# Kernel optimization log

Measured on AMD Instinct MI355X. Metric: run time of the kernel, lower is better.

Reference implementation:

```python
import jax, jax.numpy as jnp
import numpy as np
import math

N = 60000          # nodes per node type
M = 60000          # edges per edge type
H = 64             # hidden_dim
PE = 4             # pe_dim
L = 3              # message passing layers
E = 24             # edge types
PE_LEN = 2 * N     # pe table length = 2 * num_pick_nodes
T = 6              # node types: object, ssBox, place_frame, ssCylinder, pick, place

# (src_type, dst_type) index per edge type, following detailed_edge_types order
SRC = np.array([0,1,2,1,2,0,4,5,0,1,2,3,0,4,2,4,3,4,0,5,3,5,2,5])
DST = np.array([1,0,1,2,0,2,5,4,0,1,2,3,4,0,4,2,4,3,5,0,5,3,5,2])


def posenc(n, d):
    pos = jnp.arange(n, dtype=jnp.float32)[:, None]
    div = jnp.exp(jnp.arange(0, d, 2, dtype=jnp.float32) * (-math.log(10000.0) / d))
    ang = pos * div  # [n, d//2]
    return jnp.stack([jnp.sin(ang), jnp.cos(ang)], axis=-1).reshape(n, d)


def setup_inputs():
    key = jax.random.key(0)
    ks = iter(jax.random.split(key, 48))
    def n_(shape, fan):
        return jax.random.normal(next(ks), shape, dtype=jnp.float32) / np.sqrt(fan).astype(np.float32)
    def ti(shape, hi):
        return jax.random.randint(next(ks), shape, 0, hi, dtype=jnp.int32)
    inp = {}
    inp['x_object'] = jax.random.normal(next(ks), (N, 4), dtype=jnp.float32)
    inp['x_ssBox'] = jax.random.normal(next(ks), (N, 4), dtype=jnp.float32)
    inp['x_place_frame'] = jax.random.normal(next(ks), (N, 4), dtype=jnp.float32)
    inp['x_ssCylinder'] = jax.random.normal(next(ks), (N, 3), dtype=jnp.float32)
    for nt in ['object', 'ssBox', 'place_frame', 'ssCylinder', 'pick', 'place']:
        inp['times_' + nt] = ti((N,), PE_LEN)
    inp['edge_index'] = ti((E, 2, M), N)
    inp['W_object'] = n_((8, H), 8); inp['b_object'] = jnp.zeros((H,), jnp.float32)
    inp['W_ssBox'] = n_((8, H), 8); inp['b_ssBox'] = jnp.zeros((H,), jnp.float32)
    inp['W_place_frame'] = n_((8, H), 8); inp['b_place_frame'] = jnp.zeros((H,), jnp.float32)
    inp['W_ssCylinder'] = n_((7, H), 7); inp['b_ssCylinder'] = jnp.zeros((H,), jnp.float32)
    inp['W_pick'] = n_((PE, H), PE); inp['b_pick'] = jnp.zeros((H,), jnp.float32)
    inp['W_place'] = n_((PE, H), PE); inp['b_place'] = jnp.zeros((H,), jnp.float32)
    inp['Wl'] = n_((L, E, H, H), H)
    inp['bl'] = jnp.zeros((L, E, H), jnp.float32)
    inp['Wr'] = n_((L, E, H, H), H)
    inp['Wm1'] = n_((H, H // 4), H); inp['bm1'] = jnp.zeros((H // 4,), jnp.float32)
    inp['Wm2'] = n_((H // 4, 1), H // 4); inp['bm2'] = jnp.zeros((1,), jnp.float32)
    return inp


def _forward(x_object, x_ssBox, x_place_frame, x_ssCylinder,
             W_object, b_object, W_ssBox, b_ssBox, W_place_frame, b_place_frame,
             W_ssCylinder, b_ssCylinder, W_pick, b_pick, W_place, b_place,
             Wl, bl, Wr, Wm1, bm1, Wm2, bm2,
             times_object, times_ssBox, times_place_frame, times_ssCylinder,
             times_pick, times_place, edge_index):
    pe = posenc(PE_LEN, PE)
    def emb(x, t, W, b):  # features || pe[times] -> linear
        return jnp.concatenate([x, pe[t]], axis=1) @ W + b
    X = jnp.stack([
        emb(x_object, times_object, W_object, b_object),
        emb(x_ssBox, times_ssBox, W_ssBox, b_ssBox),
        emb(x_place_frame, times_place_frame, W_place_frame, b_place_frame),
        emb(x_ssCylinder, times_ssCylinder, W_ssCylinder, b_ssCylinder),
        pe[times_pick] @ W_pick + b_pick,    # constraint nodes: pe -> linear
        pe[times_place] @ W_place + b_place,
    ])  # [T, N, H]

    src_e = edge_index[:, 0]  # [E, M]
    dst_e = edge_index[:, 1]  # [E, M]
    seg_sum = jax.vmap(lambda v, s: jax.ops.segment_sum(v, s, num_segments=N))
    counts = seg_sum(jnp.ones((E, M), jnp.float32), dst_e)  # [E, N] in-degree per edge type
    denom = jnp.maximum(counts, 1.0)[..., None]

    for l in range(L):
        # gather src node states per edge type: [E, M, H]
        msgs = jnp.take_along_axis(X[SRC], src_e[..., None], axis=1)
        # mean aggregation into dst nodes per edge type (SAGEConv aggr='mean')
        agg = seg_sum(msgs, dst_e) / denom  # [E, N, H]
        # out = lin_l(agg) + lin_r(x_dst) per edge type
        out_et = (jnp.einsum('enh,ehk->enk', agg, Wl[l]) + bl[l][:, None, :]
                  + jnp.einsum('enh,ehk->enk', X[DST], Wr[l]))  # [E, N, H]
        # sum contributions across edge types sharing a dst node type
        X = jax.ops.segment_sum(out_et, DST, num_segments=T)
        X = jax.nn.relu(X)

    # pool constraint (pick/place) node embeddings into a graph embedding
    graph_emb = X[4].sum(axis=0) + X[5].sum(axis=0)  # [H]
    h = jax.nn.relu(graph_emb)          # OutputMLP: act, (dropout=id), linear
    h = jax.nn.relu(h @ Wm1 + bm1)
    return h @ Wm2 + bm2                # [output_dim]


def reference(x_object, x_ssBox, x_place_frame, x_ssCylinder,
              times_object, times_ssBox, times_place_frame, times_ssCylinder,
              times_pick, times_place, edge_index,
              W_object, b_object, W_ssBox, b_ssBox, W_place_frame, b_place_frame,
              W_ssCylinder, b_ssCylinder, W_pick, b_pick, W_place, b_place,
              Wl, bl, Wr, Wm1, bm1, Wm2, bm2):
    return _forward(x_object, x_ssBox, x_place_frame, x_ssCylinder,
                    W_object, b_object, W_ssBox, b_ssBox, W_place_frame, b_place_frame,
                    W_ssCylinder, b_ssCylinder, W_pick, b_pick, W_place, b_place,
                    Wl, bl, Wr, Wm1, bm1, Wm2, bm2,
                    times_object, times_ssBox, times_place_frame, times_ssCylinder,
                    times_pick, times_place, edge_index)
```

## Files before the change

kernel.cpp:

```cpp
#include <hip/hip_runtime.h>


#define NN 60000
#define MM 60000
#define EE 24
#define TT 6
#define NTILES ((NN + 63) / 64)
#define SCH 2048
#define SNB ((NN + SCH - 1) / SCH)
#define CSRCAP 180

typedef unsigned short u16;
typedef unsigned int   u32;
typedef __attribute__((ext_vector_type(8))) short bf16x8;
typedef __attribute__((ext_vector_type(4))) float f32x4;

__constant__ int c_SRC[EE] = {0,1,2,1,2,0,4,5,0,1,2,3,0,4,2,4,3,4,0,5,3,5,2,5};
__constant__ int c_ELIST[TT][5] = {{1,4,8,13,19},{0,2,9,0,0},{3,5,10,15,23},
                                   {11,17,21,0,0},{7,12,14,16,0},{6,18,20,22,0}};
__constant__ int c_ECOUNT[TT] = {5,3,5,3,4,4};
__constant__ int c_TLIST[3][6] = {{0,1,2,3,4,5},{0,2,3,4,5,0},{4,5,0,0,0,0}};

__device__ __forceinline__ float lo16(u32 u){ union{u32 i; float f;} x; x.i = u << 16; return x.f; }
__device__ __forceinline__ float hi16(u32 u){ union{u32 i; float f;} x; x.i = u & 0xFFFF0000u; return x.f; }
__device__ __forceinline__ float bf2f(u16 u){ union{u32 i; float f;} x; x.i = (u32)u << 16; return x.f; }
__device__ __forceinline__ u16 f2bf(float f){
  union{float f; u32 i;} x; x.f = f;
  u32 r = (x.i + 0x7FFFu + ((x.i >> 16) & 1u)) >> 16;
  return (u16)r;
}
__device__ __forceinline__ u32 pack2(float a, float b){ return (u32)f2bf(a) | ((u32)f2bf(b) << 16); }

__global__ __launch_bounds__(256) void k_prep(const float* __restrict__ Wl, const float* __restrict__ bl,
                                              const float* __restrict__ Wr,
                                              u16* __restrict__ WlT, u16* __restrict__ WrTs,
                                              float* __restrict__ blsum)
{
  const int total1 = 3*EE*4096, total2 = 3*TT*4096, total3 = 3*TT*64;
  for (int i = blockIdx.x*blockDim.x + threadIdx.x; i < total1+total2+total3; i += gridDim.x*blockDim.x) {
    if (i < total1) {
      int h = i & 63, ko = (i >> 6) & 63, le = i >> 12;
      WlT[i] = f2bf(Wl[(size_t)le*4096 + h*64 + ko]);
    } else if (i < total1 + total2) {
      int j = i - total1;
      int h = j & 63, ko = (j >> 6) & 63, lt = j >> 12;
      int l = lt / TT, t = lt % TT;
      float s = 0.f;
      for (int q = 0; q < c_ECOUNT[t]; ++q) {
        int e = c_ELIST[t][q];
        s += Wr[((size_t)(l*EE + e)*64 + h)*64 + ko];
      }
      WrTs[j] = f2bf(s);
    } else {
      int j = i - total1 - total2;
      int k = j & 63, lt = j >> 6;
      int l = lt / TT, t = lt % TT;
      float s = 0.f;
      for (int q = 0; q < c_ECOUNT[t]; ++q) s += bl[(size_t)(l*EE + c_ELIST[t][q])*64 + k];
      blsum[j] = s;
    }
  }
}

__global__ __launch_bounds__(256) void k_pe(
    const int* __restrict__ tm0, const int* __restrict__ tm1,
    const int* __restrict__ tm2, const int* __restrict__ tm3,
    const int* __restrict__ tm4, const int* __restrict__ tm5,
    float4* __restrict__ pe)
{
  const int i = blockIdx.x*blockDim.x + threadIdx.x;
  if (i >= TT*NN) return;
  const int t = i / NN, n = i - t*NN;
  int tm;
  switch (t) {
    case 0:  tm = tm0[n]; break;
    case 1:  tm = tm1[n]; break;
    case 2:  tm = tm2[n]; break;
    case 3:  tm = tm3[n]; break;
    case 4:  tm = tm4[n]; break;
    default: tm = tm5[n]; break;
  }
  const float a0 = (float)tm, a1 = a0 * 0.01f;
  float4 v;
  v.x = sinf(a0); v.y = cosf(a0); v.z = sinf(a1); v.w = cosf(a1);
  pe[i] = v;
}

__global__ __launch_bounds__(256) void k_embed(
    const float* __restrict__ x0, const float* __restrict__ x1,
    const float* __restrict__ x2, const float* __restrict__ x3,
    const float4* __restrict__ pe,
    const float* __restrict__ W0, const float* __restrict__ b0,
    const float* __restrict__ W1, const float* __restrict__ b1,
    const float* __restrict__ W2, const float* __restrict__ b2,
    const float* __restrict__ W3, const float* __restrict__ b3,
    const float* __restrict__ W4, const float* __restrict__ b4,
    const float* __restrict__ W5, const float* __restrict__ b5,
    u16* __restrict__ X)
{
  const int tid = threadIdx.x;
  const int t = blockIdx.y;
  const int n = blockIdx.x * 4 + (tid >> 6);
  const int k = tid & 63;
  const float4 p = pe[(size_t)t*NN + n];
  const float p0 = p.x, p1 = p.y, p2 = p.z, p3 = p.w;
  float acc;
  if (t == 0) {
    const float* x = x0 + (size_t)n*4;
    acc = b0[k] + x[0]*W0[k] + x[1]*W0[64+k] + x[2]*W0[128+k] + x[3]*W0[192+k]
        + p0*W0[256+k] + p1*W0[320+k] + p2*W0[384+k] + p3*W0[448+k];
  } else if (t == 1) {
    const float* x = x1 + (size_t)n*4;
    acc = b1[k] + x[0]*W1[k] + x[1]*W1[64+k] + x[2]*W1[128+k] + x[3]*W1[192+k]
        + p0*W1[256+k] + p1*W1[320+k] + p2*W1[384+k] + p3*W1[448+k];
  } else if (t == 2) {
    const float* x = x2 + (size_t)n*4;
    acc = b2[k] + x[0]*W2[k] + x[1]*W2[64+k] + x[2]*W2[128+k] + x[3]*W2[192+k]
        + p0*W2[256+k] + p1*W2[320+k] + p2*W2[384+k] + p3*W2[448+k];
  } else if (t == 3) {
    const float* x = x3 + (size_t)n*3;
    acc = b3[k] + x[0]*W3[k] + x[1]*W3[64+k] + x[2]*W3[128+k]
        + p0*W3[192+k] + p1*W3[256+k] + p2*W3[320+k] + p3*W3[384+k];
  } else if (t == 4) {
    acc = b4[k] + p0*W4[k] + p1*W4[64+k] + p2*W4[128+k] + p3*W4[192+k];
  } else {
    acc = b5[k] + p0*W5[k] + p1*W5[64+k] + p2*W5[128+k] + p3*W5[192+k];
  }
  X[((size_t)t*NN + n)*64 + k] = f2bf(acc);
}

__global__ __launch_bounds__(256) void k_count(const int* __restrict__ ei, int* __restrict__ counts) {
  for (int i = blockIdx.x*blockDim.x + threadIdx.x; i < EE*MM; i += gridDim.x*blockDim.x) {
    int e = i / MM, m = i - e*MM;
    int d = ei[(size_t)e*2*MM + MM + m];
    atomicAdd(&counts[(size_t)e*NN + d], 1);
  }
}

__global__ __launch_bounds__(256) void k_scan1(const int* __restrict__ counts, int* __restrict__ ctot) {
  const int e = blockIdx.y, ch = blockIdx.x;
  const int tid = threadIdx.x, lane = tid & 63, wid = tid >> 6;
  __shared__ int ws[4];
  int s = 0;
  for (int i = tid; i < SCH; i += 256) {
    int n = ch*SCH + i;
    if (n < NN) s += counts[(size_t)e*NN + n];
  }
  #pragma unroll
  for (int d = 1; d < 64; d <<= 1) s += __shfl_xor(s, d);
  if (lane == 0) ws[wid] = s;
  __syncthreads();
  if (tid == 0) ctot[e*SNB + ch] = ws[0] + ws[1] + ws[2] + ws[3];
}

__global__ __launch_bounds__(64) void k_scan2(int* __restrict__ ctot) {
  const int e = blockIdx.x, lane = threadIdx.x;
  int v = (lane < SNB) ? ctot[e*SNB + lane] : 0;
  int s = v;
  #pragma unroll
  for (int d = 1; d < 64; d <<= 1) { int u = __shfl_up(s, d); if (lane >= d) s += u; }
  if (lane < SNB) ctot[e*SNB + lane] = s - v;
}

__global__ __launch_bounds__(256) void k_scan3(const int* __restrict__ counts, const int* __restrict__ ctot,
                                               int* __restrict__ offs) {
  const int e = blockIdx.y, ch = blockIdx.x;
  const int tid = threadIdx.x, lane = tid & 63, wid = tid >> 6;
  __shared__ int ws[4];
  __shared__ int cbase;
  if (tid == 0) cbase = ctot[e*SNB + ch];
  __syncthreads();
  for (int i0 = 0; i0 < SCH; i0 += 256) {
    const int n = ch*SCH + i0 + tid;
    const int c = (n < NN) ? counts[(size_t)e*NN + n] : 0;
    int s = c;
    #pragma unroll
    for (int d = 1; d < 64; d <<= 1) { int u = __shfl_up(s, d); if (lane >= d) s += u; }
    if (lane == 63) ws[wid] = s;
    __syncthreads();
    int wbase = 0;
    for (int q = 0; q < wid; ++q) wbase += ws[q];
    if (n < NN) offs[(size_t)e*(NN+1) + n] = cbase + wbase + s - c;
    __syncthreads();
    if (tid == 0) cbase += ws[0] + ws[1] + ws[2] + ws[3];
    __syncthreads();
  }
  if (ch == SNB-1 && tid == 0) offs[(size_t)e*(NN+1) + NN] = cbase;
}

__global__ __launch_bounds__(256) void k_place(const int* __restrict__ ei, const int* __restrict__ offs,
                                               int* __restrict__ counts, int* __restrict__ csr) {
  for (int i = blockIdx.x*blockDim.x + threadIdx.x; i < EE*MM; i += gridDim.x*blockDim.x) {
    int e = i / MM, m = i - e*MM;
    int s = ei[(size_t)e*2*MM + m];
    int d = ei[(size_t)e*2*MM + MM + m];
    int old = atomicSub(&counts[(size_t)e*NN + d], 1);
    csr[(size_t)e*MM + offs[(size_t)e*(NN+1) + d] + old - 1] = s;
  }
}

struct WB { int offs_w[65]; int csr_w[CSRCAP]; };

__device__ __forceinline__ void mm_tile(f32x4 acc[4], const u16* la, const u16* lb, int lane, int w)
{
  const int arow = w*16 + (lane & 15);
  const int kel  = (lane >> 4) * 8;
  #pragma unroll
  for (int kb = 0; kb < 2; ++kb) {
    bf16x8 a = *(const bf16x8*)&la[arow*72 + kb*32 + kel];
    #pragma unroll
    for (int nt = 0; nt < 4; ++nt) {
      bf16x8 b = *(const bf16x8*)&lb[(nt*16 + (lane & 15))*72 + kb*32 + kel];
      acc[nt] = __builtin_amdgcn_mfma_f32_16x16x32_bf16(a, b, acc[nt], 0, 0, 0);
    }
  }
}

__global__ __launch_bounds__(256) void k_layer(
    const u16* __restrict__ Xin, u16* __restrict__ Xout,
    const int* __restrict__ offs, const int* __restrict__ csr,
    const u16* __restrict__ WlT, const u16* __restrict__ WrTs,
    const float* __restrict__ blsum, float* __restrict__ gemb, int l)
{
  __shared__ __align__(16) u16 lds_a[64*72];
  __shared__ __align__(16) u16 lds_b[64*72];
  __shared__ WB wbuf[2];
  __shared__ int ph_beg[8], ph_cnt[8];

  const int tid  = threadIdx.x;
  const int tile = blockIdx.x % NTILES;
  const int t    = c_TLIST[l][blockIdx.x / NTILES];
  const int n0   = tile * 64;
  const int lane = tid & 63;
  const int w    = tid >> 6;
  const int ec   = c_ECOUNT[t];

  if (tid < ec) {
    const int e2 = c_ELIST[t][tid];
    int hi = n0 + 64; if (hi > NN) hi = NN;
    int b  = offs[(size_t)e2*(NN+1) + n0];
    int en = offs[(size_t)e2*(NN+1) + hi];
    ph_beg[tid+1] = b; ph_cnt[tid+1] = en - b;
  }
  __syncthreads();

  auto stage_win = [&](int qp) {
    if (qp > ec) return;
    const int e2 = c_ELIST[t][qp-1];
    WB* w2 = &wbuf[qp & 1];
    const int beg2 = ph_beg[qp], cnt2 = ph_cnt[qp];
    if (tid < 65) {
      int idx = n0 + tid; if (idx > NN) idx = NN;
      w2->offs_w[tid] = offs[(size_t)e2*(NN+1) + idx] - beg2;
    }
    const int lim = cnt2 < CSRCAP ? cnt2 : CSRCAP;
    for (int i = tid; i < lim; i += 256) w2->csr_w[i] = csr[(size_t)e2*MM + beg2 + i];
  };

  f32x4 acc[4];
  #pragma unroll
  for (int i = 0; i < 4; ++i) acc[i] = (f32x4){0.f,0.f,0.f,0.f};

  {
    stage_win(1);
    const int r = tid >> 2, h0 = (tid & 3) * 16;
    const int n = n0 + r;
    uint4 v0 = {0,0,0,0}, v1 = {0,0,0,0};
    if (n < NN) {
      const uint4* p = (const uint4*)(Xin + ((size_t)t*NN + n)*64 + h0);
      v0 = p[0]; v1 = p[1];
    }
    *(uint4*)&lds_a[r*72 + h0]     = v0;
    *(uint4*)&lds_a[r*72 + h0 + 8] = v1;
    const uint4* q = (const uint4*)(WrTs + (size_t)(l*TT + t)*4096 + r*64 + h0);
    uint4 w0 = q[0], w1 = q[1];
    *(uint4*)&lds_b[r*72 + h0]     = w0;
    *(uint4*)&lds_b[r*72 + h0 + 8] = w1;
  }
  __syncthreads();
  mm_tile(acc, lds_a, lds_b, lane, w);

  for (int qq = 1; qq <= ec; ++qq) {
    const int e = c_ELIST[t][qq-1];
    const int s = c_SRC[e];
    __syncthreads();
    stage_win(qq + 1);
    {
      const WB* wb = &wbuf[qq & 1];
      const int beg = ph_beg[qq], cnt = ph_cnt[qq];
      const int r = tid >> 2;
      const int h0 = (tid & 3) * 16;
      const int n = n0 + r;
      const u16* Xs = Xin + (size_t)s * NN * 64;
      float a[16];
      #pragma unroll
      for (int i = 0; i < 16; ++i) a[i] = 0.f;
      if (n < NN) {
        const int b  = wb->offs_w[r];
        const int en = wb->offs_w[r+1];
        if (cnt <= CSRCAP) {
          int j = b; int sn; uint4 v0, v1;
          if (j < en) {
            sn = wb->csr_w[j];
            const u16* xp = Xs + (size_t)sn*64 + h0;
            v0 = *(const uint4*)xp; v1 = *(const uint4*)(xp + 8);
          }
          while (j < en) {
            uint4 c0 = v0, c1 = v1;
            ++j;
            if (j < en) {
              sn = wb->csr_w[j];
              const u16* xp = Xs + (size_t)sn*64 + h0;
              v0 = *(const uint4*)xp; v1 = *(const uint4*)(xp + 8);
            }
            a[0]+=lo16(c0.x); a[1]+=hi16(c0.x); a[2]+=lo16(c0.y); a[3]+=hi16(c0.y);
            a[4]+=lo16(c0.z); a[5]+=hi16(c0.z); a[6]+=lo16(c0.w); a[7]+=hi16(c0.w);
            a[8]+=lo16(c1.x); a[9]+=hi16(c1.x); a[10]+=lo16(c1.y); a[11]+=hi16(c1.y);
            a[12]+=lo16(c1.z); a[13]+=hi16(c1.z); a[14]+=lo16(c1.w); a[15]+=hi16(c1.w);
          }
        } else {
          for (int j = b; j < en; ++j) {
            int sn = csr[(size_t)e*MM + beg + j];
            const u16* xp = Xs + (size_t)sn*64 + h0;
            uint4 c0 = *(const uint4*)xp, c1 = *(const uint4*)(xp + 8);
            a[0]+=lo16(c0.x); a[1]+=hi16(c0.x); a[2]+=lo16(c0.y); a[3]+=hi16(c0.y);
            a[4]+=lo16(c0.z); a[5]+=hi16(c0.z); a[6]+=lo16(c0.w); a[7]+=hi16(c0.w);
            a[8]+=lo16(c1.x); a[9]+=hi16(c1.x); a[10]+=lo16(c1.y); a[11]+=hi16(c1.y);
            a[12]+=lo16(c1.z); a[13]+=hi16(c1.z); a[14]+=lo16(c1.w); a[15]+=hi16(c1.w);
          }
        }
        const int d = en - b;
        const float rd = 1.0f / (float)(d > 1 ? d : 1);
        #pragma unroll
        for (int i = 0; i < 16; ++i) a[i] *= rd;
      }
      uint4 s0, s1;
      s0.x = pack2(a[0],a[1]);   s0.y = pack2(a[2],a[3]);
      s0.z = pack2(a[4],a[5]);   s0.w = pack2(a[6],a[7]);
      s1.x = pack2(a[8],a[9]);   s1.y = pack2(a[10],a[11]);
      s1.z = pack2(a[12],a[13]); s1.w = pack2(a[14],a[15]);
      *(uint4*)&lds_a[r*72 + h0]     = s0;
      *(uint4*)&lds_a[r*72 + h0 + 8] = s1;
    }
    {
      const int r2 = tid >> 2, g0 = (tid & 3) * 16;
      const uint4* p = (const uint4*)(WlT + (size_t)(l*EE + e)*4096 + r2*64 + g0);
      uint4 w0 = p[0], w1 = p[1];
      *(uint4*)&lds_b[r2*72 + g0]     = w0;
      *(uint4*)&lds_b[r2*72 + g0 + 8] = w1;
    }
    __syncthreads();
    mm_tile(acc, lds_a, lds_b, lane, w);
  }

  __syncthreads();
  {
    const int col = lane & 15;
    const int rb  = w*16 + ((lane >> 4) << 2);
    #pragma unroll
    for (int nt = 0; nt < 4; ++nt) {
      const float blv = blsum[(size_t)(l*TT + t)*64 + nt*16 + col];
      #pragma unroll
      for (int j = 0; j < 4; ++j) {
        const float v = fmaxf(acc[nt][j] + blv, 0.f);
        const int rl = rb + j;
        lds_a[rl*72 + nt*16 + col] = ((n0 + rl) < NN) ? f2bf(v) : (u16)0;
      }
    }
  }
  __syncthreads();
  if (l < 2) {
    const int r = tid >> 2, h0 = (tid & 3) * 16;
    const int n = n0 + r;
    if (n < NN) {
      uint4 v0 = *(const uint4*)&lds_a[r*72 + h0];
      uint4 v1 = *(const uint4*)&lds_a[r*72 + h0 + 8];
      uint4* dst = (uint4*)(Xout + ((size_t)t*NN + n)*64 + h0);
      dst[0] = v0; dst[1] = v1;
    }
  } else if (tid < 64) {
    float sm = 0.f;
    for (int r = 0; r < 64; ++r) sm += bf2f(lds_a[r*72 + tid]);
    atomicAdd(&gemb[tid], sm);
  }
}

__global__ void k_head(const float* __restrict__ gemb, const float* __restrict__ Wm1,
                       const float* __restrict__ bm1, const float* __restrict__ Wm2,
                       const float* __restrict__ bm2, float* __restrict__ out)
{
  __shared__ float h[64];
  __shared__ float h2[16];
  const int tid = threadIdx.x;
  if (tid < 64) h[tid] = fmaxf(gemb[tid], 0.f);
  __syncthreads();
  if (tid < 16) {
    float a = bm1[tid];
    for (int i = 0; i < 64; ++i) a += h[i] * Wm1[i*16 + tid];
    h2[tid] = fmaxf(a, 0.f);
  }
  __syncthreads();
  if (tid == 0) {
    float a = bm2[0];
    for (int j = 0; j < 16; ++j) a += h2[j] * Wm2[j];
    out[0] = a;
  }
}

extern "C" void kernel_launch(void* const* d_in, const int* in_sizes, int n_in,
                              void* d_out, int out_size, void* d_ws, size_t ws_size,
                              hipStream_t stream) {
  char* ws = (char*)d_ws;
  size_t off = 0;
  auto take = [&](size_t bytes) -> char* {
    char* p = ws + off;
    off += (bytes + 255) & ~(size_t)255;
    return p;
  };
  u16*   XA     = (u16*)  take((size_t)6*NN*64*2);
  u16*   XB     = (u16*)  take((size_t)6*NN*64*2);
  u16*   WlT    = (u16*)  take((size_t)3*EE*4096*2);
  u16*   WrTs   = (u16*)  take((size_t)3*TT*4096*2);
  float* blsum  = (float*)take((size_t)3*TT*64*4);
  int*   counts = (int*)  take((size_t)EE*NN*4);
  int*   offs   = (int*)  take((size_t)EE*(NN+1)*4);
  int*   csr    = (int*)  take((size_t)EE*MM*4);
  int*   ctot   = (int*)  take((size_t)EE*SNB*4);
  float* petab  = (float*)take((size_t)TT*NN*16);
  float* gemb   = (float*)take(64*4);
  (void)ws_size; (void)in_sizes; (void)n_in; (void)out_size;

  hipMemsetAsync(counts, 0, (size_t)EE*NN*4, stream);
  hipMemsetAsync(gemb, 0, 64*4, stream);

  const float* Wl = (const float*)d_in[23];
  const float* bl = (const float*)d_in[24];
  const float* Wr = (const float*)d_in[25];

  k_prep<<<512, 256, 0, stream>>>(Wl, bl, Wr, WlT, WrTs, blsum);

  k_pe<<<(TT*NN + 255)/256, 256, 0, stream>>>(
      (const int*)d_in[4], (const int*)d_in[5], (const int*)d_in[6],
      (const int*)d_in[7], (const int*)d_in[8], (const int*)d_in[9],
      (float4*)petab);

  k_embed<<<dim3(NN/4, 6), 256, 0, stream>>>(
      (const float*)d_in[0], (const float*)d_in[1], (const float*)d_in[2], (const float*)d_in[3],
      (const float4*)petab,
      (const float*)d_in[11], (const float*)d_in[12],
      (const float*)d_in[13], (const float*)d_in[14],
      (const float*)d_in[15], (const float*)d_in[16],
      (const float*)d_in[17], (const float*)d_in[18],
      (const float*)d_in[19], (const float*)d_in[20],
      (const float*)d_in[21], (const float*)d_in[22],
      XA);

  const int* ei = (const int*)d_in[10];
  k_count<<<2048, 256, 0, stream>>>(ei, counts);
  k_scan1<<<dim3(SNB, EE), 256, 0, stream>>>(counts, ctot);
  k_scan2<<<EE, 64, 0, stream>>>(ctot);
  k_scan3<<<dim3(SNB, EE), 256, 0, stream>>>(counts, ctot, offs);
  k_place<<<2048, 256, 0, stream>>>(ei, offs, counts, csr);

  k_layer<<<NTILES*6, 256, 0, stream>>>(XA, XB, offs, csr, WlT, WrTs, blsum, gemb, 0);
  k_layer<<<NTILES*5, 256, 0, stream>>>(XB, XA, offs, csr, WlT, WrTs, blsum, gemb, 1);
  k_layer<<<NTILES*2, 256, 0, stream>>>(XA, XB, offs, csr, WlT, WrTs, blsum, gemb, 2);

  k_head<<<1, 64, 0, stream>>>(gemb, (const float*)d_in[26], (const float*)d_in[27],
                               (const float*)d_in[28], (const float*)d_in[29], (float*)d_out);
}
```

Baseline: 541.8 us.

## Parallelize neighbor aggregation over edges with LDS float atomics

Replaces the per-destination-row gather loop, where 4 threads walk one row's neighbor list, with an edge-parallel scheme. Each 8-thread group handles one edge, finds its destination row by binary search over the windowed offsets, and atomically adds the 8 feature values into an fp32 LDS accumulator. A separate pass then applies the mean scaling, packs to bf16, and clears the accumulator. The aim is to remove load imbalance from skewed degrees and expose more memory-level parallelism, at the cost of LDS atomics, an extra barrier, and about 17KB more shared memory, which may lower occupancy.

```diff
diff --git a/kernel.cpp b/kernel.cpp
--- a/kernel.cpp
+++ b/kernel.cpp
@@ -224,6 +224,7 @@
 {
   __shared__ __align__(16) u16 lds_a[64*72];
   __shared__ __align__(16) u16 lds_b[64*72];
+  __shared__ __align__(16) float aggf[64*68];
   __shared__ WB wbuf[2];
   __shared__ int ph_beg[8], ph_cnt[8];
 
@@ -241,6 +242,12 @@
     int b  = offs[(size_t)e2*(NN+1) + n0];
     int en = offs[(size_t)e2*(NN+1) + hi];
     ph_beg[tid+1] = b; ph_cnt[tid+1] = en - b;
+  }
+
+  {
+    float4 z = {0.f,0.f,0.f,0.f};
+    float4* az = (float4*)aggf;
+    for (int i = tid; i < 64*68/4; i += 256) az[i] = z;
   }
   __syncthreads();
 
@@ -288,59 +295,30 @@
     {
       const WB* wb = &wbuf[qq & 1];
       const int beg = ph_beg[qq], cnt = ph_cnt[qq];
-      const int r = tid >> 2;
-      const int h0 = (tid & 3) * 16;
-      const int n = n0 + r;
+      const int h0 = (tid & 7) * 8;
+      const int eb = tid >> 3;
       const u16* Xs = Xin + (size_t)s * NN * 64;
-      float a[16];
-      #pragma unroll
-      for (int i = 0; i < 16; ++i) a[i] = 0.f;
-      if (n < NN) {
-        const int b  = wb->offs_w[r];
-        const int en = wb->offs_w[r+1];
-        if (cnt <= CSRCAP) {
-          int j = b; int sn; uint4 v0, v1;
-          if (j < en) {
-            sn = wb->csr_w[j];
-            const u16* xp = Xs + (size_t)sn*64 + h0;
-            v0 = *(const uint4*)xp; v1 = *(const uint4*)(xp + 8);
+      const bool inLds = (cnt <= CSRCAP);
+      for (int jb = 0; jb < cnt; jb += 32) {
+        const int j = jb + eb;
+        if (j < cnt) {
+          const int sn = inLds ? wb->csr_w[j] : csr[(size_t)e*MM + beg + j];
+          const uint4 v = *(const uint4*)(Xs + (size_t)sn*64 + h0);
+          int lo = 0, hi = 64;
+          #pragma unroll
+          for (int st = 0; st < 6; ++st) {
+            const int mid = (lo + hi) >> 1;
+            const bool ge = (wb->offs_w[mid] <= j);
+            lo = ge ? mid : lo;
+            hi = ge ? hi : mid;
           }
-          while (j < en) {
-            uint4 c0 = v0, c1 = v1;
-            ++j;
-            if (j < en) {
-              sn = wb->csr_w[j];
-              const u16* xp = Xs + (size_t)sn*64 + h0;
-              v0 = *(const uint4*)xp; v1 = *(const uint4*)(xp + 8);
-            }
-            a[0]+=lo16(c0.x); a[1]+=hi16(c0.x); a[2]+=lo16(c0.y); a[3]+=hi16(c0.y);
-            a[4]+=lo16(c0.z); a[5]+=hi16(c0.z); a[6]+=lo16(c0.w); a[7]+=hi16(c0.w);
-            a[8]+=lo16(c1.x); a[9]+=hi16(c1.x); a[10]+=lo16(c1.y); a[11]+=hi16(c1.y);
-            a[12]+=lo16(c1.z); a[13]+=hi16(c1.z); a[14]+=lo16(c1.w); a[15]+=hi16(c1.w);
-          }
-        } else {
-          for (int j = b; j < en; ++j) {
-            int sn = csr[(size_t)e*MM + beg + j];
-            const u16* xp = Xs + (size_t)sn*64 + h0;
-            uint4 c0 = *(const uint4*)xp, c1 = *(const uint4*)(xp + 8);
-            a[0]+=lo16(c0.x); a[1]+=hi16(c0.x); a[2]+=lo16(c0.y); a[3]+=hi16(c0.y);
-            a[4]+=lo16(c0.z); a[5]+=hi16(c0.z); a[6]+=lo16(c0.w); a[7]+=hi16(c0.w);
-            a[8]+=lo16(c1.x); a[9]+=hi16(c1.x); a[10]+=lo16(c1.y); a[11]+=hi16(c1.y);
-            a[12]+=lo16(c1.z); a[13]+=hi16(c1.z); a[14]+=lo16(c1.w); a[15]+=hi16(c1.w);
-          }
+          float* ap = &aggf[lo*68 + h0];
+          atomicAdd(ap+0, lo16(v.x)); atomicAdd(ap+1, hi16(v.x));
+          atomicAdd(ap+2, lo16(v.y)); atomicAdd(ap+3, hi16(v.y));
+          atomicAdd(ap+4, lo16(v.z)); atomicAdd(ap+5, hi16(v.z));
+          atomicAdd(ap+6, lo16(v.w)); atomicAdd(ap+7, hi16(v.w));
         }
-        const int d = en - b;
-        const float rd = 1.0f / (float)(d > 1 ? d : 1);
-        #pragma unroll
-        for (int i = 0; i < 16; ++i) a[i] *= rd;
       }
-      uint4 s0, s1;
-      s0.x = pack2(a[0],a[1]);   s0.y = pack2(a[2],a[3]);
-      s0.z = pack2(a[4],a[5]);   s0.w = pack2(a[6],a[7]);
-      s1.x = pack2(a[8],a[9]);   s1.y = pack2(a[10],a[11]);
-      s1.z = pack2(a[12],a[13]); s1.w = pack2(a[14],a[15]);
-      *(uint4*)&lds_a[r*72 + h0]     = s0;
-      *(uint4*)&lds_a[r*72 + h0 + 8] = s1;
     }
     {
       const int r2 = tid >> 2, g0 = (tid & 3) * 16;
@@ -348,6 +326,24 @@
       uint4 w0 = p[0], w1 = p[1];
       *(uint4*)&lds_b[r2*72 + g0]     = w0;
       *(uint4*)&lds_b[r2*72 + g0 + 8] = w1;
+    }
+    __syncthreads();
+    {
+      const WB* wb = &wbuf[qq & 1];
+      const int r = tid >> 2, g0 = (tid & 3) * 16;
+      const int deg = wb->offs_w[r+1] - wb->offs_w[r];
+      const float rd = 1.0f / (float)(deg > 1 ? deg : 1);
+      float4* ap4 = (float4*)&aggf[r*68 + g0];
+      float4 b0 = ap4[0], b1 = ap4[1], b2 = ap4[2], b3 = ap4[3];
+      float4 z = {0.f,0.f,0.f,0.f};
+      ap4[0] = z; ap4[1] = z; ap4[2] = z; ap4[3] = z;
+      uint4 s0, s1;
+      s0.x = pack2(b0.x*rd, b0.y*rd); s0.y = pack2(b0.z*rd, b0.w*rd);
+      s0.z = pack2(b1.x*rd, b1.y*rd); s0.w = pack2(b1.z*rd, b1.w*rd);
+      s1.x = pack2(b2.x*rd, b2.y*rd); s1.y = pack2(b2.z*rd, b2.w*rd);
+      s1.z = pack2(b3.x*rd, b3.y*rd); s1.w = pack2(b3.z*rd, b3.w*rd);
+      *(uint4*)&lds_a[r*72 + g0]     = s0;
+      *(uint4*)&lds_a[r*72 + g0 + 8] = s1;
     }
     __syncthreads();
     mm_tile(acc, lds_a, lds_b, lane, w);
```

Result: slower. 1.561 ms (+188.1%).
